# Kernel optimization log

Hardware: AMD Instinct MI355X
Metric: run time of the kernel (lower is better)

Reference implementation:

```python
import jax, jax.numpy as jnp
import numpy as np

B, S, D = 2, 2048, 4096
NQ, NKV, DK = 32, 4, 128
GROUPS = NQ // NKV  # 8
NEG = -1e9  # finite stand-in for -inf so fully-masked rows stay NaN-free


def setup_inputs() -> dict:
    key = jax.random.key(0)
    ks = jax.random.split(key, 5)
    return {
        "x": jax.random.normal(ks[0], (B, S, D), jnp.float32),
        "Wq": jax.random.normal(ks[1], (D, NQ * DK), jnp.float32) * 0.02,
        "Wk": jax.random.normal(ks[2], (D, NKV * DK), jnp.float32) * 0.02,
        "Wv": jax.random.normal(ks[3], (D, NKV * DK), jnp.float32) * 0.02,
        "Wo": jax.random.normal(ks[4], (NQ * DK, D), jnp.float32) * 0.02,
    }


def reference(x, Wq, Wk, Wv, Wo):
    b, s, _ = x.shape
    # projections -> [b, heads, s, dk]
    Q = (x @ Wq).reshape(b, s, NQ, DK).transpose(0, 2, 1, 3)
    K = (x @ Wk).reshape(b, s, NKV, DK).transpose(0, 2, 1, 3)
    V = (x @ Wv).reshape(b, s, NKV, DK).transpose(0, 2, 1, 3)
    # GQA: repeat_interleave KV heads to match Q heads
    K = jnp.repeat(K, GROUPS, axis=1)  # [b, NQ, s, dk]
    V = jnp.repeat(V, GROUPS, axis=1)
    scores = jnp.einsum("bhqd,bhkd->bhqk", Q, K) / np.sqrt(DK).astype(np.float32)
    # faithful to source: mask = triu(ones(s, kv_len), diag=kv_len-s+1); fill where mask==0
    mask = jnp.triu(jnp.ones((s, s), jnp.float32), k=1)
    scores = jnp.where(mask == 0, NEG, scores)
    attn = jax.nn.softmax(scores, axis=-1)  # dropout = identity (eval)
    out = jnp.einsum("bhqk,bhkd->bhqd", attn, V)
    out = out.transpose(0, 2, 1, 3).reshape(b, s, NQ * DK)
    return out @ Wo
```

## Files before the change

kernel.cpp:

```cpp
#include <hip/hip_runtime.h>
#include <hip/hip_bf16.h>

#define S_LEN 2048
#define DMODEL 4096
#define NQH 32
#define NKVH 4
#define DKH 128

typedef __attribute__((ext_vector_type(8))) short bf16x8;
typedef __attribute__((ext_vector_type(4))) float f32x4;

union PU { unsigned u[4]; bf16x8 v; };

__device__ __forceinline__ float b2f(short u) {
  union { float f; unsigned int i; } cv;
  cv.i = ((unsigned int)(unsigned short)u) << 16;
  return cv.f;
}

__device__ __forceinline__ unsigned cvt_pk(float lo, float hi) {
  unsigned r;
  asm("v_cvt_pk_bf16_f32 %0, %1, %2" : "=v"(r) : "v"(lo), "v"(hi));
  return r;
}

__device__ __forceinline__ void gload16(const void* g, void* l) {
  __builtin_amdgcn_global_load_lds(
      (const __attribute__((address_space(1))) void*)g,
      (__attribute__((address_space(3))) void*)l, 16, 0, 0);
}

#define BAR()                         \
  {                                   \
    asm volatile("" ::: "memory");    \
    __builtin_amdgcn_s_barrier();     \
    asm volatile("" ::: "memory");    \
  }

__global__ __launch_bounds__(256) void cast_kernel(
    const float* __restrict__ in, __hip_bfloat16* __restrict__ out, int n4) {
  for (int i = blockIdx.x * 256 + threadIdx.x; i < n4; i += gridDim.x * 256) {
    const float4 v = reinterpret_cast<const float4*>(in)[i];
    __hip_bfloat16 t[4] = {__float2bfloat16(v.x), __float2bfloat16(v.y),
                           __float2bfloat16(v.z), __float2bfloat16(v.w)};
    reinterpret_cast<uint2*>(out)[i] = *reinterpret_cast<const uint2*>(t);
  }
}

__global__ __launch_bounds__(256) void transpose_cast_kernel(
    const float* __restrict__ W, __hip_bfloat16* __restrict__ WT, int K, int N) {
  __shared__ __align__(16) __hip_bfloat16 tile[64][64];
  const int tid = threadIdx.x;
  const int n0 = blockIdx.x * 64, k0 = blockIdx.y * 64;
#pragma unroll
  for (int i = 0; i < 2; ++i) {
    const int fid = i * 256 + tid;
    const int r = fid >> 3, cc = fid & 7;
    const float4 v0 = *reinterpret_cast<const float4*>(
        &W[(size_t)(k0 + r) * N + n0 + cc * 8]);
    const float4 v1 = *reinterpret_cast<const float4*>(
        &W[(size_t)(k0 + r) * N + n0 + cc * 8 + 4]);
    __hip_bfloat16 t[8] = {__float2bfloat16(v0.x), __float2bfloat16(v0.y),
                           __float2bfloat16(v0.z), __float2bfloat16(v0.w),
                           __float2bfloat16(v1.x), __float2bfloat16(v1.y),
                           __float2bfloat16(v1.z), __float2bfloat16(v1.w)};
    *reinterpret_cast<bf16x8*>(&tile[r][(cc ^ (r & 7)) << 3]) =
        *reinterpret_cast<const bf16x8*>(t);
  }
  __syncthreads();
  const int n = tid >> 2, kw = tid & 3;
#pragma unroll
  for (int i = 0; i < 2; ++i) {
    const int kc = kw + i * 4;
    __hip_bfloat16 t[8];
#pragma unroll
    for (int j = 0; j < 8; ++j) {
      const int r = kc * 8 + j;
      t[j] = tile[r][((((n >> 3) ^ (r & 7)) << 3)) + (n & 7)];
    }
    *reinterpret_cast<bf16x8*>(&WT[(size_t)(n0 + n) * K + k0 + kc * 8]) =
        *reinterpret_cast<const bf16x8*>(t);
  }
}

template <int WMODE>
__global__ __launch_bounds__(512, 2) void gemm256(
    const __hip_bfloat16* __restrict__ A, const __hip_bfloat16* __restrict__ BT,
    void* __restrict__ C) {
  __shared__ __align__(16) char ldsA[131072];
  const char* lds = &ldsA[0];
  const int tid = threadIdx.x, lane = tid & 63, w = tid >> 6;
  const int l15 = lane & 15, g = lane >> 4;
  const int wr = w >> 2, wcn = w & 3;
  const int id = blockIdx.x;
  const int swz = (id & 7) * 32 + (id >> 3);
  const int bm = (swz >> 4) * 256, bn = (swz & 15) * 256;
  const int row0 = tid >> 3;
  const int kbg = ((tid & 7) * 16) ^ ((row0 & 7) << 4);
  const char* Ab = (const char*)A;
  const char* Bb = (const char*)BT;
  const size_t aR = (size_t)(bm + row0) * 8192 + kbg;
  const size_t bR = (size_t)(bn + row0) * 8192 + kbg;
  char* ldsw = const_cast<char*>(lds) + w * 1024;
  const int sw = (l15 & 7) << 4;
  const int okk = (g * 16) ^ sw;
  const int rA = (wr * 64 + l15) * 128;
  const int rB = (wcn * 32 + l15) * 128;

  f32x4 acc[8][4] = {};

#define STG2(XR, XB, DST)            \
  gload16(XB + (XR), ldsw + (DST));  \
  gload16(XB + (XR) + 524288, ldsw + (DST) + 8192)

  STG2(aR, Ab, 0);
  STG2(bR, Bb, 65536);
  STG2(aR + 1048576, Ab, 16384);
  STG2(bR + 1048576, Bb, 65536 + 16384);
  STG2(aR + 128, Ab, 32768);
  STG2(bR + 128, Bb, 65536 + 32768);

  for (int t = 0; t < 64; ++t) {
    const int pc = t & 1, pn = pc ^ 1;
    const int pA = pc * 32768, pB = 65536 + pc * 32768;
    const size_t s01 = (size_t)((t + 1 < 64) ? t + 1 : t - 1) * 128;
    const size_t s23 = (size_t)((t + 2 < 64) ? t + 2 : t) * 128;
    asm volatile("s_waitcnt vmcnt(4)" ::: "memory");
    BAR();
    bf16x8 a0[4][2], b0[2][2];
#pragma unroll
    for (int m = 0; m < 4; ++m)
#pragma unroll
      for (int kk = 0; kk < 2; ++kk)
        a0[m][kk] = *reinterpret_cast<const bf16x8*>(
            lds + pA + rA + m * 2048 + (okk ^ (kk << 6)));
#pragma unroll
    for (int n = 0; n < 2; ++n)
#pragma unroll
      for (int kk = 0; kk < 2; ++kk)
        b0[n][kk] = *reinterpret_cast<const bf16x8*>(
            lds + pB + rB + n * 2048 + (okk ^ (kk << 6)));
    STG2(aR + 1048576 + s01, Ab, pn * 32768 + 16384);
    BAR();
    __builtin_amdgcn_s_setprio(1);
#pragma unroll
    for (int kk = 0; kk < 2; ++kk)
#pragma unroll
      for (int m = 0; m < 4; ++m)
#pragma unroll
        for (int n = 0; n < 2; ++n)
          acc[m][n] = __builtin_amdgcn_mfma_f32_16x16x32_bf16(
              a0[m][kk], b0[n][kk], acc[m][n], 0, 0, 0);
    __builtin_amdgcn_s_setprio(0);
    bf16x8 b1[2][2];
#pragma unroll
    for (int n = 0; n < 2; ++n)
#pragma unroll
      for (int kk = 0; kk < 2; ++kk)
        b1[n][kk] = *reinterpret_cast<const bf16x8*>(
            lds + pB + 16384 + rB + n * 2048 + (okk ^ (kk << 6)));
    STG2(bR + 1048576 + s01, Bb, 65536 + pn * 32768 + 16384);
    BAR();
    __builtin_amdgcn_s_setprio(1);
#pragma unroll
    for (int kk = 0; kk < 2; ++kk)
#pragma unroll
      for (int m = 0; m < 4; ++m)
#pragma unroll
        for (int n = 0; n < 2; ++n)
          acc[m][2 + n] = __builtin_amdgcn_mfma_f32_16x16x32_bf16(
              a0[m][kk], b1[n][kk], acc[m][2 + n], 0, 0, 0);
    __builtin_amdgcn_s_setprio(0);
    bf16x8 a1[4][2];
#pragma unroll
    for (int m = 0; m < 4; ++m)
#pragma unroll
      for (int kk = 0; kk < 2; ++kk)
        a1[m][kk] = *reinterpret_cast<const bf16x8*>(
            lds + pA + 16384 + rA + m * 2048 + (okk ^ (kk << 6)));
    STG2(aR + s23, Ab, pc * 32768);
    BAR();
    __builtin_amdgcn_s_setprio(1);
#pragma unroll
    for (int kk = 0; kk < 2; ++kk)
#pragma unroll
      for (int m = 0; m < 4; ++m)
#pragma unroll
        for (int n = 0; n < 2; ++n)
          acc[4 + m][n] = __builtin_amdgcn_mfma_f32_16x16x32_bf16(
              a1[m][kk], b0[n][kk], acc[4 + m][n], 0, 0, 0);
    __builtin_amdgcn_s_setprio(0);
    STG2(bR + s23, Bb, 65536 + pc * 32768);
    __builtin_amdgcn_s_setprio(1);
#pragma unroll
    for (int kk = 0; kk < 2; ++kk)
#pragma unroll
      for (int m = 0; m < 4; ++m)
#pragma unroll
        for (int n = 0; n < 2; ++n)
          acc[4 + m][2 + n] = __builtin_amdgcn_mfma_f32_16x16x32_bf16(
              a1[m][kk], b1[n][kk], acc[4 + m][2 + n], 0, 0, 0);
    __builtin_amdgcn_s_setprio(0);
  }
  asm volatile("s_waitcnt vmcnt(0)" ::: "memory");

  const int crow0 = bm + wr * 64 + g * 4;
  const int ccol0 = bn + wcn * 32 + l15;
#pragma unroll
  for (int M = 0; M < 8; ++M)
#pragma unroll
    for (int N = 0; N < 4; ++N) {
      const int row = crow0 + (M >> 2) * 128 + (M & 3) * 16;
      const int col = ccol0 + (N >> 1) * 128 + (N & 1) * 16;
#pragma unroll
      for (int r = 0; r < 4; ++r) {
        if constexpr (WMODE == 0)
          ((float*)C)[(size_t)(row + r) * 4096 + col] = acc[M][N][r];
        else
          ((__hip_bfloat16*)C)[(size_t)(row + r) * 4096 + col] =
              __float2bfloat16(acc[M][N][r]);
      }
    }
}

__global__ __launch_bounds__(256) void gemm_kv(
    const __hip_bfloat16* __restrict__ A, const __hip_bfloat16* __restrict__ BT,
    __hip_bfloat16* __restrict__ Kb, __hip_bfloat16* __restrict__ VT) {
  __shared__ __align__(16) __hip_bfloat16 As[64 * 32];
  __shared__ __align__(16) __hip_bfloat16 Bs[128 * 32];
  const int tid = threadIdx.x, lane = tid & 63, w = tid >> 6;
  const int l15 = lane & 15, l4 = lane >> 4;
  const int bm = blockIdx.y * 64, bn = blockIdx.x * 128;
  const int wr = (w >> 1) * 32, wc = (w & 1) * 64;
  const int srow = lane >> 2, scol = (lane & 3) * 8;
  const __hip_bfloat16* ga = &A[(size_t)(bm + (tid >> 2)) * 4096 + scol];
  const __hip_bfloat16* gb = &BT[(size_t)(bn + w * 16 + srow) * 4096 + scol];
  char* laA = (char*)&As[0] + w * 1024;
  char* lb0 = (char*)&Bs[0] + w * 1024;
  char* lb1 = (char*)&Bs[0] + 4096 + w * 1024;
  f32x4 acc[2][4] = {};

  for (int k0 = 0; k0 < 4096; k0 += 32) {
    gload16(ga, laA);
    gload16(gb, lb0);
    gload16(gb + (size_t)64 * 4096, lb1);
    ga += 32;
    gb += 32;
    __syncthreads();
    bf16x8 af[2], bfr[4];
#pragma unroll
    for (int m = 0; m < 2; ++m)
      af[m] = *reinterpret_cast<const bf16x8*>(
          &As[(wr + m * 16 + l15) * 32 + l4 * 8]);
#pragma unroll
    for (int n = 0; n < 4; ++n)
      bfr[n] = *reinterpret_cast<const bf16x8*>(
          &Bs[(wc + n * 16 + l15) * 32 + l4 * 8]);
#pragma unroll
    for (int m = 0; m < 2; ++m)
#pragma unroll
      for (int n = 0; n < 4; ++n)
        acc[m][n] = __builtin_amdgcn_mfma_f32_16x16x32_bf16(af[m], bfr[n],
                                                            acc[m][n], 0, 0, 0);
    __syncthreads();
  }

#pragma unroll
  for (int m = 0; m < 2; ++m)
#pragma unroll
    for (int n = 0; n < 4; ++n)
#pragma unroll
      for (int r = 0; r < 4; ++r) {
        const int row = bm + wr + m * 16 + l4 * 4 + r;
        const int col = bn + wc + n * 16 + l15;
        const __hip_bfloat16 v = __float2bfloat16(acc[m][n][r]);
        if (col < 512) {
          Kb[(size_t)row * 512 + col] = v;
        } else {
          const int b = row >> 11, s = row & 2047;
          VT[(size_t)(b * 512 + (col - 512)) * 2048 + s] = v;
        }
      }
}

__global__ __launch_bounds__(512, 4) void attn_kernel(
    const __hip_bfloat16* __restrict__ Q, const __hip_bfloat16* __restrict__ Kb,
    const __hip_bfloat16* __restrict__ VT, __hip_bfloat16* __restrict__ O) {
  __shared__ __align__(16) __hip_bfloat16 Kbuf[2][64 * 128];
  __shared__ __align__(16) __hip_bfloat16 Vbuf[2][128 * 64];
  const int tid = threadIdx.x, lane = tid & 63, w = tid >> 6;
  const int l15 = lane & 15, g = (lane >> 4) & 3;
  const int d = blockIdx.x;
  const int xg = d & 7, hh = (d >> 3) & 7, pr = d >> 6;
  const int bh = xg * 8 + hh;
  const int b = bh >> 5, h = bh & 31, kvh = (bh & 31) >> 3;
  const char* kbase = (const char*)Kb + (size_t)(b * S_LEN) * 1024 + kvh * 256;
  const char* vbase = (const char*)VT + (size_t)(b * 512 + kvh * 128) * 4096;
  const __hip_bfloat16* qbase =
      Q + (size_t)(b * S_LEN) * DMODEL + (size_t)h * DKH;
  __hip_bfloat16* obase = O + (size_t)(b * S_LEN) * DMODEL + (size_t)h * DKH;
  const int krr = lane >> 4, kcb = (lane & 15) * 16;
  const int vrr = lane >> 3, vcb = (lane & 7) * 16;
  char* klds = (char*)&Kbuf[0][0] + w * 2048;
  char* vlds = (char*)&Vbuf[0][0] + w * 2048;
  const int swr = (l15 & 7) * 16;
  const int sl_lo = l15 + ((g & 1) << 5);
  const int sl_hi = sl_lo + 16;
  const bool hi = (g & 2) != 0;
  const float SCL2 = 0.12751742f;

  int par = 0;
  for (int ph = 0; ph < 2; ++ph) {
    const int pp = ph ? (15 - pr) : pr;
    const int qw = pp * 128 + w * 16;
    const int qa = qw + l15;
    bf16x8 qf[4];
#pragma unroll
    for (int kb = 0; kb < 4; ++kb)
      qf[kb] = *reinterpret_cast<const bf16x8*>(
          &qbase[(size_t)(qw + l15) * DMODEL + kb * 32 + g * 8]);
    float lsum = 0.f;
    f32x4 oacc[8] = {};
    const int t0 = pp * 2;
    {
      const int kv0 = t0 * 64;
#pragma unroll
      for (int i = 0; i < 2; ++i) {
        const int rr = 8 * w + 4 * i + krr;
        gload16(kbase + (size_t)(kv0 + rr) * 1024 + (kcb ^ ((rr & 7) * 16)),
                klds + par * 16384 + i * 1024);
        const int r2 = 16 * w + 8 * i + vrr;
        gload16(vbase + (size_t)r2 * 4096 + kv0 * 2 + (vcb ^ ((r2 & 7) * 16)),
                vlds + par * 16384 + i * 1024);
      }
    }
    for (int t = t0; t < 32; ++t) {
      __syncthreads();
      if (t + 1 < 32) {
        const int kv0 = (t + 1) * 64;
        const int np = par ^ 1;
#pragma unroll
        for (int i = 0; i < 2; ++i) {
          const int rr = 8 * w + 4 * i + krr;
          gload16(kbase + (size_t)(kv0 + rr) * 1024 + (kcb ^ ((rr & 7) * 16)),
                  klds + np * 16384 + i * 1024);
          const int r2 = 16 * w + 8 * i + vrr;
          gload16(vbase + (size_t)r2 * 4096 + kv0 * 2 + (vcb ^ ((r2 & 7) * 16)),
                  vlds + np * 16384 + i * 1024);
        }
      }
      const char* kp = (const char*)&Kbuf[0][0] + par * 16384;
      const char* vp = (const char*)&Vbuf[0][0] + par * 16384;
      f32x4 sT[4];
#pragma unroll
      for (int c = 0; c < 4; ++c) {
        f32x4 s = {};
#pragma unroll
        for (int kb = 0; kb < 4; ++kb) {
          const bf16x8 kf = *reinterpret_cast<const bf16x8*>(
              kp + (16 * c + l15) * 256 + ((kb * 64 + g * 16) ^ swr));
          s = __builtin_amdgcn_mfma_f32_16x16x32_bf16(kf, qf[kb], s, 0, 0, 0);
        }
        sT[c] = s;
      }
#pragma unroll
      for (int c = 0; c < 4; ++c)
#pragma unroll
        for (int r = 0; r < 4; ++r)
          sT[c][r] = __builtin_amdgcn_exp2f(fmaf(sT[c][r], SCL2, -16.f));
      if (t < t0 + 2) {
        const int dthr = qa - t * 64 - 4 * g;
#pragma unroll
        for (int c = 0; c < 4; ++c)
#pragma unroll
          for (int r = 0; r < 4; ++r)
            if (16 * c + r <= dthr) sT[c][r] = 0.f;
      }
#pragma unroll
      for (int c = 0; c < 4; ++c)
#pragma unroll
        for (int r = 0; r < 4; ++r) lsum += sT[c][r];
      unsigned P0[4], P1[4];
#pragma unroll
      for (int c = 0; c < 4; ++c) {
        P0[c] = cvt_pk(sT[c][0], sT[c][1]);
        P1[c] = cvt_pk(sT[c][2], sT[c][3]);
      }
#pragma unroll
      for (int ks = 0; ks < 2; ++ks) {
        const int a0 = (int)P0[2 * ks], a1 = (int)P1[2 * ks];
        const int b0 = (int)P0[2 * ks + 1], b1 = (int)P1[2 * ks + 1];
        const unsigned s0a = __shfl(a0, sl_lo), s0b = __shfl(b0, sl_lo);
        const unsigned s1a = __shfl(a1, sl_lo), s1b = __shfl(b1, sl_lo);
        const unsigned s2a = __shfl(a0, sl_hi), s2b = __shfl(b0, sl_hi);
        const unsigned s3a = __shfl(a1, sl_hi), s3b = __shfl(b1, sl_hi);
        PU pu;
        pu.u[0] = hi ? s0b : s0a;
        pu.u[1] = hi ? s1b : s1a;
        pu.u[2] = hi ? s2b : s2a;
        pu.u[3] = hi ? s3b : s3a;
#pragma unroll
        for (int n = 0; n < 8; ++n) {
          const bf16x8 vf = *reinterpret_cast<const bf16x8*>(
              vp + (16 * n + l15) * 128 + ((ks * 64 + g * 16) ^ swr));
          oacc[n] =
              __builtin_amdgcn_mfma_f32_16x16x32_bf16(vf, pu.v, oacc[n], 0, 0, 0);
        }
      }
      par ^= 1;
    }
    lsum += __shfl_xor(lsum, 16);
    lsum += __shfl_xor(lsum, 32);
    const float rinv = 1.f / lsum;
    __hip_bfloat16* orow = obase + (size_t)(qw + l15) * DMODEL;
#pragma unroll
    for (int n = 0; n < 8; ++n) {
      uint2 st;
      st.x = cvt_pk(oacc[n][0] * rinv, oacc[n][1] * rinv);
      st.y = cvt_pk(oacc[n][2] * rinv, oacc[n][3] * rinv);
      *reinterpret_cast<uint2*>(&orow[16 * n + 4 * g]) = st;
    }
    __syncthreads();
  }
}

__global__ __launch_bounds__(128) void fixup_kernel(
    const __hip_bfloat16* __restrict__ VT, __hip_bfloat16* __restrict__ O) {
  const int b = blockIdx.x >> 5;
  const int h = blockIdx.x & 31;
  const int kvh = h >> 3;
  const int dk = threadIdx.x;
  const __hip_bfloat16* row = &VT[(size_t)(b * 512 + kvh * DKH + dk) * S_LEN];
  float s = 0.f;
  for (int i = 0; i < S_LEN / 8; ++i) {
    const bf16x8 v = *reinterpret_cast<const bf16x8*>(&row[i * 8]);
#pragma unroll
    for (int j = 0; j < 8; ++j) s += b2f(v[j]);
  }
  O[(size_t)(b * S_LEN + S_LEN - 1) * DMODEL + h * DKH + dk] =
      __float2bfloat16(s * (1.f / S_LEN));
}

extern "C" void kernel_launch(void* const* d_in, const int* in_sizes, int n_in,
                              void* d_out, int out_size, void* d_ws,
                              size_t ws_size, hipStream_t stream) {
  (void)in_sizes; (void)n_in; (void)out_size; (void)ws_size;
  const float* x = (const float*)d_in[0];
  const float* Wq = (const float*)d_in[1];
  const float* Wk = (const float*)d_in[2];
  const float* Wv = (const float*)d_in[3];
  const float* Wo = (const float*)d_in[4];
  float* out = (float*)d_out;

  char* ws = (char*)d_ws;
  __hip_bfloat16* xb  = (__hip_bfloat16*)(ws + 0);
  __hip_bfloat16* WT0 = (__hip_bfloat16*)(ws + 33554432ull);
  __hip_bfloat16* KVT = (__hip_bfloat16*)(ws + 67108864ull);
  __hip_bfloat16* Qb  = (__hip_bfloat16*)(ws + 75497472ull);
  __hip_bfloat16* Kb  = (__hip_bfloat16*)(ws + 109051904ull);
  __hip_bfloat16* VT  = (__hip_bfloat16*)(ws + 113246208ull);
  __hip_bfloat16* AO  = xb;

  const int M = 2 * S_LEN;
  dim3 blk(256);

  cast_kernel<<<dim3(2048), blk, 0, stream>>>(x, xb, (M * DMODEL) / 4);
  transpose_cast_kernel<<<dim3(64, 64), blk, 0, stream>>>(Wq, WT0, DMODEL, DMODEL);
  gemm256<1><<<dim3(256), dim3(512), 0, stream>>>(xb, WT0, Qb);
  transpose_cast_kernel<<<dim3(8, 64), blk, 0, stream>>>(Wk, KVT, DMODEL, 512);
  transpose_cast_kernel<<<dim3(8, 64), blk, 0, stream>>>(Wv, KVT + 512ull * DMODEL, DMODEL, 512);
  gemm_kv<<<dim3(8, 64), blk, 0, stream>>>(xb, KVT, Kb, VT);
  attn_kernel<<<dim3(512), dim3(512), 0, stream>>>(Qb, Kb, VT, AO);
  fixup_kernel<<<dim3(64), dim3(128), 0, stream>>>(VT, AO);
  transpose_cast_kernel<<<dim3(64, 64), blk, 0, stream>>>(Wo, WT0, DMODEL, DMODEL);
  gemm256<0><<<dim3(256), dim3(512), 0, stream>>>(AO, WT0, out);
}
```

Measured before the change: 470.4 us.

## Switch attention to 32x32x16 MFMA with 32 query rows per wave

Rewrites the attention inner loop to use 32x32x16 bf16 MFMA tiles, giving each wave 32 query rows and each block 256 rows. The P-matrix register relayout now uses permlane32_swap instead of multiple shuffles and selects. The grid is halved to 256 blocks and launch bounds are relaxed to 2 blocks per SU. The aim is more K/V reuse per LDS load, fewer MFMA issues and less shuffle overhead, at the cost of higher register pressure, lower occupancy and fewer blocks to balance the causal workload.

New measurement: 454.9 us. -3.3%, faster.

```diff
diff --git a/kernel.cpp b/kernel.cpp
--- a/kernel.cpp
+++ b/kernel.cpp
@@ -9,6 +9,8 @@
 
 typedef __attribute__((ext_vector_type(8))) short bf16x8;
 typedef __attribute__((ext_vector_type(4))) float f32x4;
+typedef __attribute__((ext_vector_type(16))) float f32x16;
+typedef __attribute__((ext_vector_type(2))) unsigned u32x2;
 
 union PU { unsigned u[4]; bf16x8 v; };
 
@@ -283,45 +285,42 @@
       }
 }
 
-__global__ __launch_bounds__(512, 4) void attn_kernel(
+__global__ __launch_bounds__(512, 2) void attn_kernel(
     const __hip_bfloat16* __restrict__ Q, const __hip_bfloat16* __restrict__ Kb,
     const __hip_bfloat16* __restrict__ VT, __hip_bfloat16* __restrict__ O) {
   __shared__ __align__(16) __hip_bfloat16 Kbuf[2][64 * 128];
   __shared__ __align__(16) __hip_bfloat16 Vbuf[2][128 * 64];
   const int tid = threadIdx.x, lane = tid & 63, w = tid >> 6;
-  const int l15 = lane & 15, g = (lane >> 4) & 3;
+  const int l31 = lane & 31, h = lane >> 5;
   const int d = blockIdx.x;
   const int xg = d & 7, hh = (d >> 3) & 7, pr = d >> 6;
   const int bh = xg * 8 + hh;
-  const int b = bh >> 5, h = bh & 31, kvh = (bh & 31) >> 3;
+  const int b = bh >> 5, hq = bh & 31, kvh = (bh & 31) >> 3;
   const char* kbase = (const char*)Kb + (size_t)(b * S_LEN) * 1024 + kvh * 256;
   const char* vbase = (const char*)VT + (size_t)(b * 512 + kvh * 128) * 4096;
   const __hip_bfloat16* qbase =
-      Q + (size_t)(b * S_LEN) * DMODEL + (size_t)h * DKH;
-  __hip_bfloat16* obase = O + (size_t)(b * S_LEN) * DMODEL + (size_t)h * DKH;
+      Q + (size_t)(b * S_LEN) * DMODEL + (size_t)hq * DKH;
+  __hip_bfloat16* obase = O + (size_t)(b * S_LEN) * DMODEL + (size_t)hq * DKH;
   const int krr = lane >> 4, kcb = (lane & 15) * 16;
   const int vrr = lane >> 3, vcb = (lane & 7) * 16;
   char* klds = (char*)&Kbuf[0][0] + w * 2048;
   char* vlds = (char*)&Vbuf[0][0] + w * 2048;
-  const int swr = (l15 & 7) * 16;
-  const int sl_lo = l15 + ((g & 1) << 5);
-  const int sl_hi = sl_lo + 16;
-  const bool hi = (g & 2) != 0;
+  const int swr = (lane & 7) * 16;
   const float SCL2 = 0.12751742f;
 
   int par = 0;
   for (int ph = 0; ph < 2; ++ph) {
-    const int pp = ph ? (15 - pr) : pr;
-    const int qw = pp * 128 + w * 16;
-    const int qa = qw + l15;
-    bf16x8 qf[4];
-#pragma unroll
-    for (int kb = 0; kb < 4; ++kb)
-      qf[kb] = *reinterpret_cast<const bf16x8*>(
-          &qbase[(size_t)(qw + l15) * DMODEL + kb * 32 + g * 8]);
+    const int pp = ph ? (7 - pr) : pr;
+    const int qw = pp * 256 + w * 32;
+    const int qa = qw + l31;
+    bf16x8 qf[8];
+#pragma unroll
+    for (int dkb = 0; dkb < 8; ++dkb)
+      qf[dkb] = *reinterpret_cast<const bf16x8*>(
+          &qbase[(size_t)qa * DMODEL + dkb * 16 + h * 8]);
     float lsum = 0.f;
-    f32x4 oacc[8] = {};
-    const int t0 = pp * 2;
+    f32x16 oaccT[4] = {};
+    const int t0 = pp * 4;
     {
       const int kv0 = t0 * 64;
 #pragma unroll
@@ -351,75 +350,81 @@
       }
       const char* kp = (const char*)&Kbuf[0][0] + par * 16384;
       const char* vp = (const char*)&Vbuf[0][0] + par * 16384;
-      f32x4 sT[4];
-#pragma unroll
-      for (int c = 0; c < 4; ++c) {
-        f32x4 s = {};
-#pragma unroll
-        for (int kb = 0; kb < 4; ++kb) {
+      f32x16 sT[2];
+#pragma unroll
+      for (int kvb = 0; kvb < 2; ++kvb) {
+        f32x16 s = {};
+#pragma unroll
+        for (int dkb = 0; dkb < 8; ++dkb) {
           const bf16x8 kf = *reinterpret_cast<const bf16x8*>(
-              kp + (16 * c + l15) * 256 + ((kb * 64 + g * 16) ^ swr));
-          s = __builtin_amdgcn_mfma_f32_16x16x32_bf16(kf, qf[kb], s, 0, 0, 0);
+              kp + (kvb * 32 + l31) * 256 + ((dkb * 32 + h * 16) ^ swr));
+          s = __builtin_amdgcn_mfma_f32_32x32x16_bf16(kf, qf[dkb], s, 0, 0, 0);
         }
-        sT[c] = s;
-      }
-#pragma unroll
-      for (int c = 0; c < 4; ++c)
-#pragma unroll
-        for (int r = 0; r < 4; ++r)
-          sT[c][r] = __builtin_amdgcn_exp2f(fmaf(sT[c][r], SCL2, -16.f));
-      if (t < t0 + 2) {
-        const int dthr = qa - t * 64 - 4 * g;
-#pragma unroll
-        for (int c = 0; c < 4; ++c)
-#pragma unroll
-          for (int r = 0; r < 4; ++r)
-            if (16 * c + r <= dthr) sT[c][r] = 0.f;
-      }
-#pragma unroll
-      for (int c = 0; c < 4; ++c)
-#pragma unroll
-        for (int r = 0; r < 4; ++r) lsum += sT[c][r];
-      unsigned P0[4], P1[4];
-#pragma unroll
-      for (int c = 0; c < 4; ++c) {
-        P0[c] = cvt_pk(sT[c][0], sT[c][1]);
-        P1[c] = cvt_pk(sT[c][2], sT[c][3]);
-      }
-#pragma unroll
-      for (int ks = 0; ks < 2; ++ks) {
-        const int a0 = (int)P0[2 * ks], a1 = (int)P1[2 * ks];
-        const int b0 = (int)P0[2 * ks + 1], b1 = (int)P1[2 * ks + 1];
-        const unsigned s0a = __shfl(a0, sl_lo), s0b = __shfl(b0, sl_lo);
-        const unsigned s1a = __shfl(a1, sl_lo), s1b = __shfl(b1, sl_lo);
-        const unsigned s2a = __shfl(a0, sl_hi), s2b = __shfl(b0, sl_hi);
-        const unsigned s3a = __shfl(a1, sl_hi), s3b = __shfl(b1, sl_hi);
-        PU pu;
-        pu.u[0] = hi ? s0b : s0a;
-        pu.u[1] = hi ? s1b : s1a;
-        pu.u[2] = hi ? s2b : s2a;
-        pu.u[3] = hi ? s3b : s3a;
-#pragma unroll
-        for (int n = 0; n < 8; ++n) {
-          const bf16x8 vf = *reinterpret_cast<const bf16x8*>(
-              vp + (16 * n + l15) * 128 + ((ks * 64 + g * 16) ^ swr));
-          oacc[n] =
-              __builtin_amdgcn_mfma_f32_16x16x32_bf16(vf, pu.v, oacc[n], 0, 0, 0);
+        sT[kvb] = s;
+      }
+#pragma unroll
+      for (int kvb = 0; kvb < 2; ++kvb)
+#pragma unroll
+        for (int r = 0; r < 16; ++r)
+          sT[kvb][r] = __builtin_amdgcn_exp2f(fmaf(sT[kvb][r], SCL2, -16.f));
+      if (t * 64 < qw + 32) {
+#pragma unroll
+        for (int kvb = 0; kvb < 2; ++kvb)
+#pragma unroll
+          for (int r = 0; r < 16; ++r) {
+            const int kvl = (r & 3) + 8 * (r >> 2) + 4 * h;
+            if (t * 64 + kvb * 32 + kvl <= qa) sT[kvb][r] = 0.f;
+          }
+      }
+#pragma unroll
+      for (int kvb = 0; kvb < 2; ++kvb)
+#pragma unroll
+        for (int r = 0; r < 16; ++r) lsum += sT[kvb][r];
+#pragma unroll
+      for (int kvb = 0; kvb < 2; ++kvb) {
+        unsigned wv[8];
+#pragma unroll
+        for (int i = 0; i < 8; ++i)
+          wv[i] = cvt_pk(sT[kvb][2 * i], sT[kvb][2 * i + 1]);
+        const u32x2 s02 =
+            __builtin_amdgcn_permlane32_swap(wv[0], wv[2], false, false);
+        const u32x2 s13 =
+            __builtin_amdgcn_permlane32_swap(wv[1], wv[3], false, false);
+        const u32x2 s46 =
+            __builtin_amdgcn_permlane32_swap(wv[4], wv[6], false, false);
+        const u32x2 s57 =
+            __builtin_amdgcn_permlane32_swap(wv[5], wv[7], false, false);
+        PU pb1, pb2;
+        pb1.u[0] = s02[0]; pb1.u[1] = s13[0]; pb1.u[2] = s02[1]; pb1.u[3] = s13[1];
+        pb2.u[0] = s46[0]; pb2.u[1] = s57[0]; pb2.u[2] = s46[1]; pb2.u[3] = s57[1];
+#pragma unroll
+        for (int dkblk = 0; dkblk < 4; ++dkblk) {
+          const bf16x8 vf1 = *reinterpret_cast<const bf16x8*>(
+              vp + (dkblk * 32 + l31) * 128 + ((kvb * 64 + h * 16) ^ swr));
+          oaccT[dkblk] = __builtin_amdgcn_mfma_f32_32x32x16_bf16(
+              vf1, pb1.v, oaccT[dkblk], 0, 0, 0);
+          const bf16x8 vf2 = *reinterpret_cast<const bf16x8*>(
+              vp + (dkblk * 32 + l31) * 128 + ((kvb * 64 + 32 + h * 16) ^ swr));
+          oaccT[dkblk] = __builtin_amdgcn_mfma_f32_32x32x16_bf16(
+              vf2, pb2.v, oaccT[dkblk], 0, 0, 0);
         }
       }
       par ^= 1;
     }
-    lsum += __shfl_xor(lsum, 16);
     lsum += __shfl_xor(lsum, 32);
     const float rinv = 1.f / lsum;
-    __hip_bfloat16* orow = obase + (size_t)(qw + l15) * DMODEL;
-#pragma unroll
-    for (int n = 0; n < 8; ++n) {
-      uint2 st;
-      st.x = cvt_pk(oacc[n][0] * rinv, oacc[n][1] * rinv);
-      st.y = cvt_pk(oacc[n][2] * rinv, oacc[n][3] * rinv);
-      *reinterpret_cast<uint2*>(&orow[16 * n + 4 * g]) = st;
-    }
+    __hip_bfloat16* orow = obase + (size_t)qa * DMODEL;
+#pragma unroll
+    for (int dkblk = 0; dkblk < 4; ++dkblk)
+#pragma unroll
+      for (int b4 = 0; b4 < 4; ++b4) {
+        uint2 st;
+        st.x = cvt_pk(oaccT[dkblk][4 * b4 + 0] * rinv,
+                      oaccT[dkblk][4 * b4 + 1] * rinv);
+        st.y = cvt_pk(oaccT[dkblk][4 * b4 + 2] * rinv,
+                      oaccT[dkblk][4 * b4 + 3] * rinv);
+        *reinterpret_cast<uint2*>(&orow[dkblk * 32 + b4 * 8 + 4 * h]) = st;
+      }
     __syncthreads();
   }
 }
@@ -470,7 +475,7 @@
   transpose_cast_kernel<<<dim3(8, 64), blk, 0, stream>>>(Wk, KVT, DMODEL, 512);
   transpose_cast_kernel<<<dim3(8, 64), blk, 0, stream>>>(Wv, KVT + 512ull * DMODEL, DMODEL, 512);
   gemm_kv<<<dim3(8, 64), blk, 0, stream>>>(xb, KVT, Kb, VT);
-  attn_kernel<<<dim3(512), dim3(512), 0, stream>>>(Qb, Kb, VT, AO);
+  attn_kernel<<<dim3(256), dim3(512), 0, stream>>>(Qb, Kb, VT, AO);
   fixup_kernel<<<dim3(64), dim3(128), 0, stream>>>(VT, AO);
   transpose_cast_kernel<<<dim3(64, 64), blk, 0, stream>>>(Wo, WT0, DMODEL, DMODEL);
   gemm256<0><<<dim3(256), dim3(512), 0, stream>>>(AO, WT0, out);
```
